# Optimization experiments

Measured on AMD Instinct MI355X. Metric: run time of the kernel, lower is better.

Reference implementation:

```python
import jax, jax.numpy as jnp
import numpy as np

IN_F = 4096
OUT_F = 4096
Q_RANK = 2
R_RANK = 2
SCALE = 1.0
B, S = 2, 2048


def setup_inputs() -> dict:
    key = jax.random.key(0)
    ks = jax.random.split(key, 8)
    inp = jax.random.normal(ks[0], (B, S, IN_F), jnp.float32)
    # Q, R come from a QR decomposition of linear.weight.t(); random stand-ins with
    # matching shapes and O(1) scale are fine for a numerical baseline.
    Q = jax.random.normal(ks[1], (IN_F, OUT_F), jnp.float32) / np.sqrt(IN_F).astype(np.float32)
    R = jax.random.normal(ks[2], (OUT_F, OUT_F), jnp.float32) / np.sqrt(OUT_F).astype(np.float32)
    # kron_Q1/Q2 are initialized to identity in __init__ (never re-initialized);
    # add small noise so the rotation path is non-trivial.
    sq1 = IN_F // Q_RANK
    kron_Q1 = jnp.eye(sq1, dtype=jnp.float32) + 0.01 * jax.random.normal(ks[3], (sq1, sq1), jnp.float32)
    kron_Q2 = jnp.eye(Q_RANK, dtype=jnp.float32) + 0.01 * jax.random.normal(ks[4], (Q_RANK, Q_RANK), jnp.float32)
    # kron_R1/R2 use normal init with std = 1/size.
    sr1 = OUT_F // R_RANK
    kron_R1 = jax.random.normal(ks[5], (sr1, sr1), jnp.float32) / sr1
    kron_R2 = jax.random.normal(ks[6], (R_RANK, R_RANK), jnp.float32) / R_RANK
    # lambda_matrix inits to zeros; use small noise so the delta term is exercised.
    lambda_matrix = 0.01 * jax.random.normal(ks[7], (OUT_F,), jnp.float32)
    return {"input": inp, "Q": Q, "R": R, "kron_Q1": kron_Q1, "kron_Q2": kron_Q2,
            "kron_R1": kron_R1, "kron_R2": kron_R2, "lambda_matrix": lambda_matrix}


def reference(input, Q, R, kron_Q1, kron_Q2, kron_R1, kron_R2, lambda_matrix):
    rotation = jnp.kron(kron_Q1, kron_Q2)          # [in, in]
    orth = jnp.kron(kron_R1, kron_R2)              # [out, out]
    # orth @ diag(lambda) @ orth.T without materializing diag
    R_eff = R + (orth * lambda_matrix[None, :]) @ orth.T  # [out, out]
    W_t = rotation @ (Q @ R_eff)                   # [in, out]
    # F.linear(input, W_t.t()) == input @ W_t; dropout is identity in eval; bias=False
    return (input @ W_t) * SCALE
```

## Files before the change

### kernel.cpp

```cpp
#include <hip/hip_runtime.h>
#include <stdint.h>


typedef unsigned short u16;
typedef short bf16x8 __attribute__((ext_vector_type(8)));
typedef float f32x4 __attribute__((ext_vector_type(4)));

__device__ __forceinline__ u16 f2bf(float f) {
  union { float f; uint32_t u; } v; v.f = f;
  return (u16)((v.u + 0x7FFFu + ((v.u >> 16) & 1u)) >> 16);
}

__device__ __forceinline__ void store_out(float* p, float v) { *p = v; }
__device__ __forceinline__ void store_out(u16* p, float v) { *p = f2bf(v); }

__device__ __forceinline__ void gload_lds16(const u16* g, u16* l) {
  __builtin_amdgcn_global_load_lds(
      (__attribute__((address_space(1))) void*)(uintptr_t)g,
      (__attribute__((address_space(3))) void*)l, 16, 0, 0);
}

#define MFMA16(a, b, c) __builtin_amdgcn_mfma_f32_16x16x32_bf16((a), (b), (c), 0, 0, 0)

template <typename OutT>
__global__ __launch_bounds__(512, 2) void gemm256(
    const u16* __restrict__ A, const u16* __restrict__ Bt, OutT* __restrict__ C,
    int M, int N, int K, int ldC, long long sA, long long sC) {
  extern __shared__ __align__(16) u16 smem[];
  u16* ldsA = smem;
  u16* ldsB = smem + 32768;

  const int tid  = (int)threadIdx.x;
  const int lane = tid & 63;
  const int wid  = tid >> 6;
  const int wr   = wid >> 2;
  const int wc   = wid & 3;

  const int tilesX = (int)gridDim.x;
  const int tilesXY = tilesX * (int)gridDim.y;
  const int nwg = tilesXY * (int)gridDim.z;
  const int bid = ((int)blockIdx.z * (int)gridDim.y + (int)blockIdx.y) * tilesX + (int)blockIdx.x;
  const int swz = (bid & 7) * (nwg >> 3) + (bid >> 3);
  const int z   = swz / tilesXY;
  const int rem = swz % tilesXY;
  const int brow = (rem / tilesX) << 8;
  const int bcol = (rem % tilesX) << 8;
  A += (size_t)z * sA;
  C += (size_t)z * sC;

  const int lr = lane & 15, lg = lane >> 4, h = lr >> 1;
  const int sf = (lg + ((lr & 1) << 2)) ^ h;
  const int abase = wr * 8192 + h * 64 + sf * 8;
  const int bbase = (wc >> 1) * 8192 + ((wc & 1) * 32 + h) * 64 + sf * 8;

  const int kp   = (tid & 7) ^ ((tid >> 3) & 7);
  const int srow = 2 * (tid >> 3) + (kp >> 2);
  const int scol = (kp & 3) << 3;
  const size_t gA0 = (size_t)(brow + srow) * K + scol;
  const size_t gB0 = (size_t)(bcol + srow) * K + scol;
  const size_t rstep = (size_t)K << 7;
  const int sdst = wid * 512;

  const int NC = K >> 6;
  const int NI = NC >> 1;

  f32x4 acc[8][4] = {};
  bf16x8 af[4][2], bf[4][2];

#define STG_A(t, rh, ks) gload_lds16(A + gA0 + (rh) * rstep + (size_t)(t) * 64 + (ks) * 32, \
    ldsA + ((t) & 1) * 16384 + (rh) * 8192 + (ks) * 4096 + sdst)
#define STG_B(t, rh, ks) gload_lds16(Bt + gB0 + (rh) * rstep + (size_t)(t) * 64 + (ks) * 32, \
    ldsB + ((t) & 1) * 16384 + (rh) * 8192 + (ks) * 4096 + sdst)
#define VM4 asm volatile("s_waitcnt vmcnt(4)" ::: "memory")
#define VM0 asm volatile("s_waitcnt vmcnt(0)" ::: "memory")

#define PH(BUF, MH, RDA, RDB01, RDB23, N0, N1, S0, S1, TAIL) do {               \
    const u16* _pa = ldsA + (BUF) * 16384 + abase;                              \
    const u16* _pb = ldsB + (BUF) * 16384 + bbase;                              \
    if (RDA) {                                                                  \
      _Pragma("unroll")                                                         \
      for (int m = 0; m < 4; ++m) {                                             \
        af[m][0] = *(const bf16x8*)(_pa + ((MH) * 4 + m) * 512);                \
        af[m][1] = *(const bf16x8*)(_pa + ((MH) * 4 + m) * 512 + 4096);         \
      }                                                                         \
    }                                                                           \
    if (RDB01) {                                                                \
      bf[0][0] = *(const bf16x8*)(_pb);        bf[0][1] = *(const bf16x8*)(_pb + 4096);       \
      bf[1][0] = *(const bf16x8*)(_pb + 512);  bf[1][1] = *(const bf16x8*)(_pb + 512 + 4096); \
    }                                                                           \
    if (RDB23) {                                                                \
      bf[2][0] = *(const bf16x8*)(_pb + 1024); bf[2][1] = *(const bf16x8*)(_pb + 1024 + 4096); \
      bf[3][0] = *(const bf16x8*)(_pb + 1536); bf[3][1] = *(const bf16x8*)(_pb + 1536 + 4096); \
    }                                                                           \
    S0; S1;                                                                     \
    __builtin_amdgcn_s_barrier();                                               \
    asm volatile("s_waitcnt lgkmcnt(0)" ::: "memory");                          \
    __builtin_amdgcn_sched_barrier(0);                                          \
    __builtin_amdgcn_s_setprio(1);                                              \
    _Pragma("unroll")                                                           \
    for (int m = 0; m < 4; ++m) {                                               \
      acc[(MH) * 4 + m][N0] = MFMA16(af[m][0], bf[N0][0], acc[(MH) * 4 + m][N0]); \
      acc[(MH) * 4 + m][N0] = MFMA16(af[m][1], bf[N0][1], acc[(MH) * 4 + m][N0]); \
      acc[(MH) * 4 + m][N1] = MFMA16(af[m][0], bf[N1][0], acc[(MH) * 4 + m][N1]); \
      acc[(MH) * 4 + m][N1] = MFMA16(af[m][1], bf[N1][1], acc[(MH) * 4 + m][N1]); \
    }                                                                           \
    __builtin_amdgcn_s_setprio(0);                                              \
    TAIL;                                                                       \
    __builtin_amdgcn_sched_barrier(0);                                          \
    __builtin_amdgcn_s_barrier();                                               \
  } while (0)

  STG_A(0, 0, 0); STG_A(0, 0, 1); STG_A(0, 1, 0); STG_A(0, 1, 1);
  STG_B(0, 0, 0); STG_B(0, 0, 1); STG_B(0, 1, 0); STG_B(0, 1, 1);
  STG_B(1, 0, 0); STG_B(1, 0, 1); STG_B(1, 1, 0); STG_B(1, 1, 1);
  VM4;
  __builtin_amdgcn_sched_barrier(0);
  __builtin_amdgcn_s_barrier();

  for (int i = 0; i < NI - 1; ++i) {
    const int tn = 2 * i;
    PH(0, 0, 1, 1, 0, 0, 1, STG_A(tn + 1, 0, 0), STG_A(tn + 1, 0, 1), (void)0);
    PH(0, 0, 0, 0, 1, 2, 3, STG_A(tn + 1, 1, 0), STG_A(tn + 1, 1, 1), (void)0);
    PH(0, 1, 1, 0, 0, 0, 1, STG_B(tn + 2, 0, 0), STG_B(tn + 2, 0, 1), (void)0);
    PH(0, 1, 0, 0, 0, 2, 3, STG_B(tn + 2, 1, 0), STG_B(tn + 2, 1, 1), VM4);
    PH(1, 0, 1, 1, 0, 0, 1, STG_A(tn + 2, 0, 0), STG_A(tn + 2, 0, 1), (void)0);
    PH(1, 0, 0, 0, 1, 2, 3, STG_A(tn + 2, 1, 0), STG_A(tn + 2, 1, 1), (void)0);
    PH(1, 1, 1, 0, 0, 0, 1, STG_B(tn + 3, 0, 0), STG_B(tn + 3, 0, 1), (void)0);
    PH(1, 1, 0, 0, 0, 2, 3, STG_B(tn + 3, 1, 0), STG_B(tn + 3, 1, 1), VM4);
  }
  {
    PH(0, 0, 1, 1, 0, 0, 1, STG_A(NC - 1, 0, 0), STG_A(NC - 1, 0, 1), (void)0);
    PH(0, 0, 0, 0, 1, 2, 3, STG_A(NC - 1, 1, 0), STG_A(NC - 1, 1, 1), (void)0);
    PH(0, 1, 1, 0, 0, 0, 1, (void)0, (void)0, (void)0);
    PH(0, 1, 0, 0, 0, 2, 3, (void)0, (void)0, VM0);
    PH(1, 0, 1, 1, 0, 0, 1, (void)0, (void)0, (void)0);
    PH(1, 0, 0, 0, 1, 2, 3, (void)0, (void)0, (void)0);
    PH(1, 1, 1, 0, 0, 0, 1, (void)0, (void)0, (void)0);
    PH(1, 1, 0, 0, 0, 2, 3, (void)0, (void)0, (void)0);
  }

#undef PH
#undef STG_A
#undef STG_B
#undef VM4
#undef VM0

#pragma unroll
  for (int m = 0; m < 8; ++m) {
    const int r0 = brow + wr * 128 + m * 16 + lg * 4;
#pragma unroll
    for (int n = 0; n < 4; ++n) {
      const int cc = bcol + wc * 64 + n * 16 + lr;
#pragma unroll
      for (int j = 0; j < 4; ++j)
        store_out(&C[(size_t)(r0 + j) * ldC + cc], acc[m][n][j]);
    }
  }
}

__global__ void trans_kernel(const float* __restrict__ in, u16* __restrict__ out, int n) {
  __shared__ float t[32][33];
  const int bx = (int)blockIdx.x * 32, by = (int)blockIdx.y * 32;
  const int x = (int)threadIdx.x, y0 = (int)threadIdx.y;
#pragma unroll
  for (int dy = 0; dy < 32; dy += 8)
    t[y0 + dy][x] = in[(size_t)(bx + y0 + dy) * n + by + x];
  __syncthreads();
#pragma unroll
  for (int dy = 0; dy < 32; dy += 8)
    out[(size_t)(by + y0 + dy) * n + bx + x] = f2bf(t[x][y0 + dy]);
}

__global__ void transperm_kernel(const float* __restrict__ in, u16* __restrict__ out) {
  __shared__ float t[32][33];
  const int bx = (int)blockIdx.x * 32, by = (int)blockIdx.y * 32;
  const int x = (int)threadIdx.x, y0 = (int)threadIdx.y;
#pragma unroll
  for (int dy = 0; dy < 32; dy += 8)
    t[y0 + dy][x] = in[(size_t)(bx + y0 + dy) * 4096 + by + x];
  __syncthreads();
  const int r = bx + x;
  const int cp = ((r & 1) << 11) | (r >> 1);
#pragma unroll
  for (int dy = 0; dy < 32; dy += 8)
    out[(size_t)(by + y0 + dy) * 4096 + cp] = f2bf(t[x][y0 + dy]);
}

__global__ void transadd_kernel(const float* __restrict__ R, const float* __restrict__ Dsub,
                                u16* __restrict__ out) {
  __shared__ float t[32][33];
  const int bx = (int)blockIdx.x * 32, by = (int)blockIdx.y * 32;
  const int x = (int)threadIdx.x, y0 = (int)threadIdx.y;
#pragma unroll
  for (int dy = 0; dy < 32; dy += 8)
    t[y0 + dy][x] = R[(size_t)(bx + y0 + dy) * 4096 + by + x];
  __syncthreads();
  const int j = bx + x;
#pragma unroll
  for (int dy = 0; dy < 32; dy += 8) {
    const int i = by + y0 + dy;
    const int s = ((i & 1) << 1) | (j & 1);
    const float d = Dsub[(size_t)s * 4194304 + ((size_t)(i >> 1) << 11) + (j >> 1)];
    out[(size_t)i * 4096 + j] = f2bf(t[x][y0 + dy] + d);
  }
}

__global__ void scale_r1_kernel(const float* __restrict__ R1, const float* __restrict__ R2,
                                const float* __restrict__ lam,
                                u16* __restrict__ R1bf, u16* __restrict__ Asc) {
  const int idx = (int)blockIdx.x * 256 + (int)threadIdx.x;
  const int i1 = idx >> 9, k1 = (idx & 511) << 2;
  const float4 r1 = *(const float4*)(R1 + (size_t)i1 * 2048 + k1);
  const float4 l0 = *(const float4*)(lam + 2 * k1);
  const float4 l1 = *(const float4*)(lam + 2 * k1 + 4);
  const float le[4] = {l0.x, l0.z, l1.x, l1.z};
  const float lo[4] = {l0.y, l0.w, l1.y, l1.w};
  const float rv[4] = {r1.x, r1.y, r1.z, r1.w};
  ushort4 rb;
  rb.x = f2bf(r1.x); rb.y = f2bf(r1.y); rb.z = f2bf(r1.z); rb.w = f2bf(r1.w);
  *(ushort4*)(R1bf + (size_t)i1 * 2048 + k1) = rb;
#pragma unroll
  for (int s = 0; s < 4; ++s) {
    const int i2 = s >> 1, j2 = s & 1;
    const float c0 = R2[i2 * 2] * R2[j2 * 2];
    const float c1 = R2[i2 * 2 + 1] * R2[j2 * 2 + 1];
    ushort4 o;
    u16* dst = Asc + (size_t)s * 4194304 + (size_t)i1 * 2048 + k1;
    o.x = f2bf(rv[0] * (le[0] * c0 + lo[0] * c1));
    o.y = f2bf(rv[1] * (le[1] * c0 + lo[1] * c1));
    o.z = f2bf(rv[2] * (le[2] * c0 + lo[2] * c1));
    o.w = f2bf(rv[3] * (le[3] * c0 + lo[3] * c1));
    *(ushort4*)dst = o;
  }
}

__global__ void tprep_kernel(const float* __restrict__ in, const float* __restrict__ Q2,
                             u16* __restrict__ T) {
  const int idx = (int)blockIdx.x * 256 + (int)threadIdx.x;
  const int s = idx >> 9, k1 = (idx & 511) << 2;
  const float4 a = *(const float4*)(in + (size_t)s * 4096 + 2 * k1);
  const float4 b = *(const float4*)(in + (size_t)s * 4096 + 2 * k1 + 4);
  const float e[4] = {a.x, a.z, b.x, b.z};
  const float o[4] = {a.y, a.w, b.y, b.w};
  const float q00 = Q2[0], q01 = Q2[1], q10 = Q2[2], q11 = Q2[3];
  ushort4 t0, t1;
  t0.x = f2bf(e[0] * q00 + o[0] * q10); t1.x = f2bf(e[0] * q01 + o[0] * q11);
  t0.y = f2bf(e[1] * q00 + o[1] * q10); t1.y = f2bf(e[1] * q01 + o[1] * q11);
  t0.z = f2bf(e[2] * q00 + o[2] * q10); t1.z = f2bf(e[2] * q01 + o[2] * q11);
  t0.w = f2bf(e[3] * q00 + o[3] * q10); t1.w = f2bf(e[3] * q01 + o[3] * q11);
  *(ushort4*)(T + (size_t)s * 2048 + k1) = t0;
  *(ushort4*)(T + 8388608 + (size_t)s * 2048 + k1) = t1;
}

extern "C" void kernel_launch(void* const* d_in, const int* in_sizes, int n_in,
                              void* d_out, int out_size, void* d_ws, size_t ws_size,
                              hipStream_t stream) {
  const float* input = (const float*)d_in[0];
  const float* Q     = (const float*)d_in[1];
  const float* R     = (const float*)d_in[2];
  const float* Q1    = (const float*)d_in[3];
  const float* Q2    = (const float*)d_in[4];
  const float* R1    = (const float*)d_in[5];
  const float* R2    = (const float*)d_in[6];
  const float* lam   = (const float*)d_in[7];
  float* out = (float*)d_out;

  const size_t MB = 1024ull * 1024ull;
  char* ws = (char*)d_ws;
  u16* R1bf  = (u16*)(ws + 0 * MB);
  u16* Asc   = (u16*)(ws + 8 * MB);
  u16* Q1tb  = (u16*)(ws + 40 * MB);
  u16* T     = (u16*)(ws + 48 * MB);
  u16* Qtp   = (u16*)(ws + 80 * MB);
  u16* rteff = (u16*)(ws + 112 * MB);
  u16* X1p   = (u16*)(ws + 144 * MB);
  u16* X2    = Asc;
  float* Dsub = (float*)d_out;

  {
    void (*pf)(const u16*, const u16*, float*, int, int, int, int, long long, long long) = gemm256<float>;
    void (*pb)(const u16*, const u16*, u16*, int, int, int, int, long long, long long)   = gemm256<u16>;
    (void)hipFuncSetAttribute((const void*)pf, hipFuncAttributeMaxDynamicSharedMemorySize, 131072);
    (void)hipFuncSetAttribute((const void*)pb, hipFuncAttributeMaxDynamicSharedMemorySize, 131072);
  }

  const dim3 tb(32, 8);
  trans_kernel<<<dim3(64, 64), tb, 0, stream>>>(Q1, Q1tb, 2048);
  transperm_kernel<<<dim3(128, 128), tb, 0, stream>>>(Q, Qtp);
  scale_r1_kernel<<<4096, 256, 0, stream>>>(R1, R2, lam, R1bf, Asc);
  tprep_kernel<<<8192, 256, 0, stream>>>(input, Q2, T);
  gemm256<float><<<dim3(8, 8, 4), 512, 131072, stream>>>(
      Asc, R1bf, Dsub, 2048, 2048, 2048, 2048, 4194304LL, 4194304LL);
  transadd_kernel<<<dim3(128, 128), tb, 0, stream>>>(R, Dsub, rteff);
  gemm256<u16><<<dim3(8, 16, 2), 512, 131072, stream>>>(
      T, Q1tb, X1p, 4096, 2048, 2048, 4096, 8388608LL, 2048LL);
  gemm256<u16><<<dim3(16, 16, 1), 512, 131072, stream>>>(
      X1p, Qtp, X2, 4096, 4096, 4096, 4096, 0LL, 0LL);
  gemm256<float><<<dim3(16, 16, 1), 512, 131072, stream>>>(
      X2, rteff, out, 4096, 4096, 4096, 4096, 0LL, 0LL);
}
```

Before: 460.4 us.

## Factor R2 coefficients out of the orth-delta GEMM to halve batched work

The delta term orth·diag(λ)·orthᵀ was computed as four batched 2048³ GEMMs, one per R2 sub-block pair, each with R2 products folded into the scaled R1 operand. Now only two GEMMs run, one for the even and one for the odd lambda entries, and the R2 coefficient products are applied later in the transpose-add kernel as scalars. This removes half of the delta GEMM FLOPs and the extra scaled operand writes. The cost is two Dsub reads per element in the add kernel, plus a changed workspace layout.

```diff
diff --git a/kernel.cpp b/kernel.cpp
--- a/kernel.cpp
+++ b/kernel.cpp
@@ -187,7 +187,7 @@
 }
 
 __global__ void transadd_kernel(const float* __restrict__ R, const float* __restrict__ Dsub,
-                                u16* __restrict__ out) {
+                                const float* __restrict__ R2, u16* __restrict__ out) {
   __shared__ float t[32][33];
   const int bx = (int)blockIdx.x * 32, by = (int)blockIdx.y * 32;
   const int x = (int)threadIdx.x, y0 = (int)threadIdx.y;
@@ -195,43 +195,39 @@
   for (int dy = 0; dy < 32; dy += 8)
     t[y0 + dy][x] = R[(size_t)(bx + y0 + dy) * 4096 + by + x];
   __syncthreads();
+  const float r20 = R2[0], r21 = R2[1], r22 = R2[2], r23 = R2[3];
   const int j = bx + x;
+  const float cj0 = (j & 1) ? r22 : r20;
+  const float cj1 = (j & 1) ? r23 : r21;
 #pragma unroll
   for (int dy = 0; dy < 32; dy += 8) {
     const int i = by + y0 + dy;
-    const int s = ((i & 1) << 1) | (j & 1);
-    const float d = Dsub[(size_t)s * 4194304 + ((size_t)(i >> 1) << 11) + (j >> 1)];
+    const float ci0 = (i & 1) ? r22 : r20;
+    const float ci1 = (i & 1) ? r23 : r21;
+    const size_t o = ((size_t)(i >> 1) << 11) + (j >> 1);
+    const float d = ci0 * cj0 * Dsub[o] + ci1 * cj1 * Dsub[o + 4194304];
     out[(size_t)i * 4096 + j] = f2bf(t[x][y0 + dy] + d);
   }
 }
 
-__global__ void scale_r1_kernel(const float* __restrict__ R1, const float* __restrict__ R2,
-                                const float* __restrict__ lam,
-                                u16* __restrict__ R1bf, u16* __restrict__ Asc) {
+__global__ void scale_r1_kernel(const float* __restrict__ R1, const float* __restrict__ lam,
+                                u16* __restrict__ R1bf, u16* __restrict__ Ae,
+                                u16* __restrict__ Ao) {
   const int idx = (int)blockIdx.x * 256 + (int)threadIdx.x;
   const int i1 = idx >> 9, k1 = (idx & 511) << 2;
   const float4 r1 = *(const float4*)(R1 + (size_t)i1 * 2048 + k1);
   const float4 l0 = *(const float4*)(lam + 2 * k1);
   const float4 l1 = *(const float4*)(lam + 2 * k1 + 4);
-  const float le[4] = {l0.x, l0.z, l1.x, l1.z};
-  const float lo[4] = {l0.y, l0.w, l1.y, l1.w};
-  const float rv[4] = {r1.x, r1.y, r1.z, r1.w};
-  ushort4 rb;
+  const size_t off = (size_t)i1 * 2048 + k1;
+  ushort4 rb, eb, ob;
   rb.x = f2bf(r1.x); rb.y = f2bf(r1.y); rb.z = f2bf(r1.z); rb.w = f2bf(r1.w);
-  *(ushort4*)(R1bf + (size_t)i1 * 2048 + k1) = rb;
-#pragma unroll
-  for (int s = 0; s < 4; ++s) {
-    const int i2 = s >> 1, j2 = s & 1;
-    const float c0 = R2[i2 * 2] * R2[j2 * 2];
-    const float c1 = R2[i2 * 2 + 1] * R2[j2 * 2 + 1];
-    ushort4 o;
-    u16* dst = Asc + (size_t)s * 4194304 + (size_t)i1 * 2048 + k1;
-    o.x = f2bf(rv[0] * (le[0] * c0 + lo[0] * c1));
-    o.y = f2bf(rv[1] * (le[1] * c0 + lo[1] * c1));
-    o.z = f2bf(rv[2] * (le[2] * c0 + lo[2] * c1));
-    o.w = f2bf(rv[3] * (le[3] * c0 + lo[3] * c1));
-    *(ushort4*)dst = o;
-  }
+  eb.x = f2bf(r1.x * l0.x); eb.y = f2bf(r1.y * l0.z);
+  eb.z = f2bf(r1.z * l1.x); eb.w = f2bf(r1.w * l1.z);
+  ob.x = f2bf(r1.x * l0.y); ob.y = f2bf(r1.y * l0.w);
+  ob.z = f2bf(r1.z * l1.y); ob.w = f2bf(r1.w * l1.w);
+  *(ushort4*)(R1bf + off) = rb;
+  *(ushort4*)(Ae + off) = eb;
+  *(ushort4*)(Ao + off) = ob;
 }
 
 __global__ void tprep_kernel(const float* __restrict__ in, const float* __restrict__ Q2,
@@ -268,13 +264,14 @@
   const size_t MB = 1024ull * 1024ull;
   char* ws = (char*)d_ws;
   u16* R1bf  = (u16*)(ws + 0 * MB);
-  u16* Asc   = (u16*)(ws + 8 * MB);
-  u16* Q1tb  = (u16*)(ws + 40 * MB);
-  u16* T     = (u16*)(ws + 48 * MB);
-  u16* Qtp   = (u16*)(ws + 80 * MB);
-  u16* rteff = (u16*)(ws + 112 * MB);
-  u16* X1p   = (u16*)(ws + 144 * MB);
-  u16* X2    = Asc;
+  u16* Ae    = (u16*)(ws + 8 * MB);
+  u16* Ao    = (u16*)(ws + 16 * MB);
+  u16* Q1tb  = (u16*)(ws + 24 * MB);
+  u16* T     = (u16*)(ws + 32 * MB);
+  u16* Qtp   = (u16*)(ws + 64 * MB);
+  u16* rteff = (u16*)(ws + 96 * MB);
+  u16* X1p   = (u16*)(ws + 128 * MB);
+  u16* X2    = (u16*)(ws + 8 * MB);
   float* Dsub = (float*)d_out;
 
   {
@@ -287,11 +284,11 @@
   const dim3 tb(32, 8);
   trans_kernel<<<dim3(64, 64), tb, 0, stream>>>(Q1, Q1tb, 2048);
   transperm_kernel<<<dim3(128, 128), tb, 0, stream>>>(Q, Qtp);
-  scale_r1_kernel<<<4096, 256, 0, stream>>>(R1, R2, lam, R1bf, Asc);
+  scale_r1_kernel<<<4096, 256, 0, stream>>>(R1, lam, R1bf, Ae, Ao);
   tprep_kernel<<<8192, 256, 0, stream>>>(input, Q2, T);
-  gemm256<float><<<dim3(8, 8, 4), 512, 131072, stream>>>(
-      Asc, R1bf, Dsub, 2048, 2048, 2048, 2048, 4194304LL, 4194304LL);
-  transadd_kernel<<<dim3(128, 128), tb, 0, stream>>>(R, Dsub, rteff);
+  gemm256<float><<<dim3(8, 8, 2), 512, 131072, stream>>>(
+      Ae, R1bf, Dsub, 2048, 2048, 2048, 2048, 4194304LL, 4194304LL);
+  transadd_kernel<<<dim3(128, 128), tb, 0, stream>>>(R, Dsub, R2, rteff);
   gemm256<u16><<<dim3(8, 16, 2), 512, 131072, stream>>>(
       T, Q1tb, X1p, 4096, 2048, 2048, 4096, 8388608LL, 2048LL);
   gemm256<u16><<<dim3(16, 16, 1), 512, 131072, stream>>>(
```

Result: faster. 436.2 us (-5.3%).
